# Kernel tuning notes

Measured on AMD Instinct MI355X. Metric: run time of the kernel, lower is better.

## Reference

```python
import jax, jax.numpy as jnp
import numpy as np

K = 3        # kernel_size
STRIDE = 1
PAD = 1
DIL = 1


def conv2d(x, w, b, stride, pad):
    y = jax.lax.conv_general_dilated(
        x, w, window_strides=(stride, stride),
        padding=[(pad, pad), (pad, pad)],
        dimension_numbers=('NCHW', 'OIHW', 'NCHW'))
    return y + b[None, :, None, None]


def bilinear_sample(x_t, py, px):
    """x_t: [B,H,W,C]; py,px: [B,Ho,Wo] float sample coords. Zero padding outside."""
    B, H, W, C = x_t.shape
    b = jnp.arange(B)[:, None, None]
    y0 = jnp.floor(py)
    x0 = jnp.floor(px)
    wy = py - y0
    wx = px - x0
    out = jnp.zeros(py.shape + (C,), x_t.dtype)
    for dy, dx, wgt in ((0, 0, (1 - wy) * (1 - wx)),
                        (0, 1, (1 - wy) * wx),
                        (1, 0, wy * (1 - wx)),
                        (1, 1, wy * wx)):
        yy = y0 + dy
        xx = x0 + dx
        valid = (yy >= 0) & (yy < H) & (xx >= 0) & (xx < W)
        yi = jnp.clip(yy, 0, H - 1).astype(jnp.int32)
        xi = jnp.clip(xx, 0, W - 1).astype(jnp.int32)
        g = x_t[b, yi, xi]                      # [B,Ho,Wo,C] gather
        out = out + g * (wgt * valid)[..., None]
    return out


def deform_conv2d(x, offset, weight, bias):
    """torchvision-style deform_conv2d (v1, 1 offset group).
    x: [B,C,H,W]; offset: [B,2*K*K,Ho,Wo] with (dy,dx) interleaved per tap;
    weight: [O,C,K,K]; bias: [O]."""
    B, C, H, W = x.shape
    O = weight.shape[0]
    Ho, Wo = offset.shape[2], offset.shape[3]
    x_t = jnp.transpose(x, (0, 2, 3, 1))        # [B,H,W,C]
    off = offset.reshape(B, K * K, 2, Ho, Wo)   # [B,K2,(dy,dx),Ho,Wo]
    base_y = (jnp.arange(Ho) * STRIDE - PAD).astype(x.dtype)
    base_x = (jnp.arange(Wo) * STRIDE - PAD).astype(x.dtype)
    samples = []
    for k in range(K * K):                      # fixed 9-tap loop
        ki, kj = divmod(k, K)
        py = base_y[None, :, None] + ki * DIL + off[:, k, 0]   # [B,Ho,Wo]
        px = base_x[None, None, :] + kj * DIL + off[:, k, 1]
        samples.append(bilinear_sample(x_t, py, px))
    sampled = jnp.stack(samples)                # [K2,B,Ho,Wo,C]
    out = jnp.einsum('kbhwc,ock->bohw', sampled, weight.reshape(O, C, K * K))
    return out + bias[None, :, None, None]


def setup_inputs() -> dict:
    key = jax.random.key(0)
    k0, k1, k2, k3 = jax.random.split(key, 4)
    B, Cin, Cout, H, W = 8, 64, 64, 128, 128
    x = jax.random.normal(k0, (B, Cin, H, W), jnp.float32)
    # offset conv: small init so sampled offsets stay near the regular grid
    w_off = jax.random.normal(k1, (2 * K * K, Cin, K, K), jnp.float32) * 0.01
    b_off = jnp.zeros((2 * K * K,), jnp.float32)
    w = jax.random.normal(k2, (Cout, Cin, K, K), jnp.float32) * (1.0 / np.sqrt(Cin * K * K))
    b = jax.random.normal(k3, (Cout,), jnp.float32) * 0.01
    return {"x": x, "w_off": w_off, "b_off": b_off, "w": w, "b": b}


def reference(x, w_off, b_off, w, b):
    offset = conv2d(x, w_off, b_off, STRIDE, PAD)   # [B,18,Ho,Wo]
    return deform_conv2d(x, offset, w, b)           # [B,64,Ho,Wo]
```

## Files before the change

kernel.cpp:

```cpp
#include <hip/hip_runtime.h>

#define B_   8
#define C_   64
#define O_   64
#define H_   128
#define W_   128
#define HO_  128
#define WO_  128
#define K2_  9
#define MOFF 18
#define PLANE (H_*W_)
#define KTOT 576

#define BROWS 5
#define BCOLS 132
#define PSTRIDE (BROWS*BCOLS*8)

typedef short bf16x8 __attribute__((ext_vector_type(8)));
typedef float f32x16 __attribute__((ext_vector_type(16)));
typedef float f32x2  __attribute__((ext_vector_type(2)));
typedef unsigned int u32x4 __attribute__((ext_vector_type(4)));

__device__ __forceinline__ unsigned short f2bf(float f) {
    unsigned u = __float_as_uint(f);
    u += 0x7fff + ((u >> 16) & 1);
    return (unsigned short)(u >> 16);
}
__device__ __forceinline__ float bf2f(short v) {
    return __uint_as_float(((unsigned)(unsigned short)v) << 16);
}
__device__ __forceinline__ f32x2 unpk(unsigned w) {
    f32x2 r;
    r.x = __uint_as_float(w << 16);
    r.y = __uint_as_float(w & 0xffff0000u);
    return r;
}

__global__ __launch_bounds__(256) void prep_kernel(const float* __restrict__ x,
                                                   const float* __restrict__ w,
                                                   const float* __restrict__ w_off,
                                                   unsigned short* __restrict__ xt,
                                                   unsigned short* __restrict__ wbf) {
    __shared__ unsigned short T[64 * 130];
    const int tid = threadIdx.x;
    if (blockIdx.x >= B_ * H_) {
        int i = (blockIdx.x - B_ * H_) * 256 + tid;
        if (i < 96 * KTOT) {
            int o = i / KTOT, pos = i % KTOT;
            int cc = pos / 144, r = pos % 144, t = r / 16, cl = r % 16;
            int c = cc * 16 + cl;
            unsigned short v;
            if (o < O_)             v = f2bf(w[o * KTOT + c * 9 + t]);
            else if (o < O_ + MOFF) v = f2bf(w_off[(o - O_) * KTOT + c * 9 + t]);
            else                    v = 0;
            wbf[i] = v;
        }
        return;
    }
    const int b = blockIdx.x & 7;
    const int y = blockIdx.x >> 3;
    const float* src = x + (size_t)b * C_ * PLANE + y * W_;
    for (int i = tid; i < 64 * 128; i += 256) {
        int c = i >> 7, px = i & 127;
        T[c * 130 + px] = f2bf(src[c * PLANE + px]);
    }
    __syncthreads();
    for (int j = tid; j < 128 * 4; j += 256) {
        int cc = j >> 7, px = j & 127;
        unsigned short* dst = xt + ((size_t)(cc * B_ + b) * PLANE + y * W_ + px) * 16;
        ushort4 v0 = { T[(cc*16+ 0)*130+px], T[(cc*16+ 1)*130+px],
                       T[(cc*16+ 2)*130+px], T[(cc*16+ 3)*130+px] };
        ushort4 v1 = { T[(cc*16+ 4)*130+px], T[(cc*16+ 5)*130+px],
                       T[(cc*16+ 6)*130+px], T[(cc*16+ 7)*130+px] };
        ushort4 v2 = { T[(cc*16+ 8)*130+px], T[(cc*16+ 9)*130+px],
                       T[(cc*16+10)*130+px], T[(cc*16+11)*130+px] };
        ushort4 v3 = { T[(cc*16+12)*130+px], T[(cc*16+13)*130+px],
                       T[(cc*16+14)*130+px], T[(cc*16+15)*130+px] };
        *(ushort4*)(dst)      = v0;
        *(ushort4*)(dst + 4)  = v1;
        *(ushort4*)(dst + 8)  = v2;
        *(ushort4*)(dst + 12) = v3;
    }
}

__global__ __launch_bounds__(256, 4) void fused_kernel(const unsigned short* __restrict__ xt,
        const unsigned short* __restrict__ wobf, const float* __restrict__ b_off,
        const unsigned short* __restrict__ wbf, const float* __restrict__ bias,
        float* __restrict__ out) {
    __shared__ __align__(16) unsigned short band[2 * PSTRIDE];
    __shared__ float lo[MOFF * 128];
    const int tid  = threadIdx.x;
    const int id   = blockIdx.x;
    const int b    = id & 7;
    const int ho   = id >> 3;
    const int wv   = tid >> 6;
    const int lane = tid & 63;
    const int m    = lane & 31;
    const int kh   = lane >> 5;
    const int pxg  = (wv << 5) + m;

    auto stage = [&](const unsigned short* xtc, int r0, int nrows) {
        const int npos = nrows * BCOLS;
        uint4 va[3], vb[3];
        #pragma unroll
        for (int it = 0; it < 3; ++it) {
            va[it] = (uint4){0, 0, 0, 0};
            vb[it] = (uint4){0, 0, 0, 0};
            int j = tid + it * 256;
            if (j < npos) {
                int r = j / BCOLS, c = j - r * BCOLS;
                int y = ho - 2 + r0 + r, x = c - 2;
                if (((unsigned)y < (unsigned)H_) && ((unsigned)x < (unsigned)W_)) {
                    const uint4* gp = (const uint4*)(xtc + (y * W_ + x) * 16);
                    va[it] = gp[0];
                    vb[it] = gp[1];
                }
            }
        }
        #pragma unroll
        for (int it = 0; it < 3; ++it) {
            int j = tid + it * 256;
            if (j < npos) {
                int r = j / BCOLS, c = j - r * BCOLS;
                int s = ((r0 + r) * BCOLS + c) * 8;
                *(uint4*)&band[s]           = va[it];
                *(uint4*)&band[PSTRIDE + s] = vb[it];
            }
        }
    };

    f32x16 acc0 = {};
    for (int cc = 0; cc < 4; ++cc) {
        const unsigned short* xtc = xt + (size_t)(cc * B_ + b) * PLANE * 16;
        stage(xtc, 1, 3);
        __syncthreads();
        #pragma unroll
        for (int ks = 0; ks < 9; ++ks) {
            bf16x8 a = *(const bf16x8*)&wobf[m * KTOT + cc * 144 + ks * 16 + kh * 8];
            bf16x8 s = *(const bf16x8*)&band[kh * PSTRIDE +
                        ((1 + ks / 3) * BCOLS + pxg + ks % 3 + 1) * 8];
            acc0 = __builtin_amdgcn_mfma_f32_32x32x16_bf16(a, s, acc0, 0, 0, 0);
        }
        __syncthreads();
    }
    #pragma unroll
    for (int r = 0; r < 16; ++r) {
        int mo = (r & 3) + ((r >> 2) << 3) + (kh << 2);
        if (mo < MOFF) lo[mo * 128 + pxg] = acc0[r] + b_off[mo];
    }
    __syncthreads();

    f32x16 acc[2] = {};
    for (int cc = 0; cc < 4; ++cc) {
        const unsigned short* xtc = xt + (size_t)(cc * B_ + b) * PLANE * 16;
        stage(xtc, 0, 5);
        __syncthreads();
        #pragma unroll
        for (int ks = 0; ks < 9; ++ks) {
            float py  = (float)(ho - 1 + ks / 3) + lo[(2 * ks) * 128 + pxg];
            float pxc = (float)(pxg - 1 + ks % 3) + lo[(2 * ks + 1) * 128 + pxg];
            float fy = floorf(py), fx = floorf(pxc);
            float wy = py - fy,    wx = pxc - fx;
            int y0 = (int)fy, x0 = (int)fx;
            int rb = y0 - ho + 2, cb = x0 + 2;
            bool oob = ((unsigned)rb > 3u) || ((unsigned)cb > 130u);
            int rbc = min(max(rb, 0), 3), cbc = min(max(cb, 0), 130);
            const unsigned short* bp = &band[kh * PSTRIDE + (rbc * BCOLS + cbc) * 8];
            const uint4 c00 = *(const uint4*)bp;
            const uint4 c01 = *(const uint4*)(bp + 8);
            const uint4 c10 = *(const uint4*)(bp + BCOLS * 8);
            const uint4 c11 = *(const uint4*)(bp + BCOLS * 8 + 8);
            const f32x2 wx2 = { wx, wx };
            const f32x2 wy2 = { wy, wy };
            u32x4 vr;
            #pragma unroll
            for (int pq = 0; pq < 4; ++pq) {
                unsigned w00 = (pq==0)?c00.x:(pq==1)?c00.y:(pq==2)?c00.z:c00.w;
                unsigned w01 = (pq==0)?c01.x:(pq==1)?c01.y:(pq==2)?c01.z:c01.w;
                unsigned w10 = (pq==0)?c10.x:(pq==1)?c10.y:(pq==2)?c10.z:c10.w;
                unsigned w11 = (pq==0)?c11.x:(pq==1)?c11.y:(pq==2)?c11.z:c11.w;
                f32x2 a2 = unpk(w00), b2 = unpk(w01);
                f32x2 c2 = unpk(w10), d2 = unpk(w11);
                f32x2 top = a2 + wx2 * (b2 - a2);
                f32x2 bot = c2 + wx2 * (d2 - c2);
                f32x2 r2  = top + wy2 * (bot - top);
                unsigned pk;
                asm("v_cvt_pk_bf16_f32 %0, %1, %2" : "=v"(pk) : "v"(r2.x), "v"(r2.y));
                vr[pq] = pk;
            }
            bf16x8 v = __builtin_bit_cast(bf16x8, vr);
            if (__builtin_expect(__any(oob), 0)) {
                if (oob) {
                    float s8[8];
                    #pragma unroll
                    for (int j = 0; j < 8; ++j) s8[j] = 0.f;
                    #pragma unroll
                    for (int c2i = 0; c2i < 4; ++c2i) {
                        int yy = y0 + (c2i >> 1);
                        int xx = x0 + (c2i & 1);
                        bool valid = ((unsigned)yy < (unsigned)H_) && ((unsigned)xx < (unsigned)W_);
                        int yc = min(max(yy, 0), H_ - 1);
                        int xc = min(max(xx, 0), W_ - 1);
                        float wgt = ((c2i >> 1) ? wy : 1.f - wy) * ((c2i & 1) ? wx : 1.f - wx);
                        wgt = valid ? wgt : 0.f;
                        const unsigned short* rp = xtc + (yc * W_ + xc) * 16 + kh * 8;
                        bf16x8 u = *(const bf16x8*)rp;
                        #pragma unroll
                        for (int j = 0; j < 8; ++j) s8[j] += wgt * bf2f(u[j]);
                    }
                    #pragma unroll
                    for (int j = 0; j < 8; ++j) v[j] = (short)f2bf(s8[j]);
                }
            }
            bf16x8 a0 = *(const bf16x8*)&wbf[m * KTOT + cc * 144 + ks * 16 + kh * 8];
            bf16x8 a1 = *(const bf16x8*)&wbf[(32 + m) * KTOT + cc * 144 + ks * 16 + kh * 8];
            acc[0] = __builtin_amdgcn_mfma_f32_32x32x16_bf16(a0, v, acc[0], 0, 0, 0);
            acc[1] = __builtin_amdgcn_mfma_f32_32x32x16_bf16(a1, v, acc[1], 0, 0, 0);
        }
        __syncthreads();
    }

    {
        float* op = out + (size_t)b * O_ * PLANE + ho * WO_ + pxg;
        #pragma unroll
        for (int nt = 0; nt < 2; ++nt) {
            #pragma unroll
            for (int r = 0; r < 16; ++r) {
                int mo = (nt << 5) + (r & 3) + ((r >> 2) << 3) + (kh << 2);
                __builtin_nontemporal_store(acc[nt][r] + bias[mo], op + (size_t)mo * PLANE);
            }
        }
    }
}

extern "C" void kernel_launch(void* const* d_in, const int* in_sizes, int n_in,
                              void* d_out, int out_size, void* d_ws, size_t ws_size,
                              hipStream_t stream) {
    const float* x     = (const float*)d_in[0];
    const float* w_off = (const float*)d_in[1];
    const float* b_off = (const float*)d_in[2];
    const float* w     = (const float*)d_in[3];
    const float* bias  = (const float*)d_in[4];
    float* out = (float*)d_out;

    unsigned short* wbf  = (unsigned short*)d_ws;
    unsigned short* wobf = wbf + O_ * KTOT;
    unsigned short* xt   = wobf + 32 * KTOT;

    const int wblocks = (96 * KTOT + 255) / 256;
    prep_kernel <<<B_ * H_ + wblocks, 256, 0, stream>>>(x, w, w_off, xt, wbf);
    fused_kernel<<<B_ * HO_, 256, 0, stream>>>(xt, wobf, b_off, wbf, bias, out);
}
```

Before: 146.3 us.

## Prefetch next channel chunk into registers while MFMA runs; vectorize prep loads

The fused kernel now issues the global loads for the next channel chunk's halo band into registers before computing on the current chunk, then writes them to shared memory at the next iteration. This overlaps global-memory latency with MFMA and bilinear work, including a prefetch of the first deform-phase band during the last offset-conv chunk. The prep kernel reads x as float4 and pads its shared transpose buffer to 132 so the vectorized stores stay aligned. The cost is extra registers held across the compute loop, which may reduce occupancy under the 256x4 launch bound.

```diff
diff --git a/kernel.cpp b/kernel.cpp
--- a/kernel.cpp
+++ b/kernel.cpp
@@ -41,7 +41,7 @@
                                                    const float* __restrict__ w_off,
                                                    unsigned short* __restrict__ xt,
                                                    unsigned short* __restrict__ wbf) {
-    __shared__ unsigned short T[64 * 130];
+    __shared__ __align__(16) unsigned short T[64 * 132];
     const int tid = threadIdx.x;
     if (blockIdx.x >= B_ * H_) {
         int i = (blockIdx.x - B_ * H_) * 256 + tid;
@@ -59,23 +59,25 @@
     }
     const int b = blockIdx.x & 7;
     const int y = blockIdx.x >> 3;
-    const float* src = x + (size_t)b * C_ * PLANE + y * W_;
-    for (int i = tid; i < 64 * 128; i += 256) {
-        int c = i >> 7, px = i & 127;
-        T[c * 130 + px] = f2bf(src[c * PLANE + px]);
+    const float4* src4 = (const float4*)(x + (size_t)b * C_ * PLANE + y * W_);
+    for (int i = tid; i < 64 * 32; i += 256) {
+        int c = i >> 5, px4 = i & 31;
+        float4 v = src4[c * (PLANE / 4) + px4];
+        ushort4 t = { f2bf(v.x), f2bf(v.y), f2bf(v.z), f2bf(v.w) };
+        *(ushort4*)&T[c * 132 + px4 * 4] = t;
     }
     __syncthreads();
     for (int j = tid; j < 128 * 4; j += 256) {
         int cc = j >> 7, px = j & 127;
         unsigned short* dst = xt + ((size_t)(cc * B_ + b) * PLANE + y * W_ + px) * 16;
-        ushort4 v0 = { T[(cc*16+ 0)*130+px], T[(cc*16+ 1)*130+px],
-                       T[(cc*16+ 2)*130+px], T[(cc*16+ 3)*130+px] };
-        ushort4 v1 = { T[(cc*16+ 4)*130+px], T[(cc*16+ 5)*130+px],
-                       T[(cc*16+ 6)*130+px], T[(cc*16+ 7)*130+px] };
-        ushort4 v2 = { T[(cc*16+ 8)*130+px], T[(cc*16+ 9)*130+px],
-                       T[(cc*16+10)*130+px], T[(cc*16+11)*130+px] };
-        ushort4 v3 = { T[(cc*16+12)*130+px], T[(cc*16+13)*130+px],
-                       T[(cc*16+14)*130+px], T[(cc*16+15)*130+px] };
+        ushort4 v0 = { T[(cc*16+ 0)*132+px], T[(cc*16+ 1)*132+px],
+                       T[(cc*16+ 2)*132+px], T[(cc*16+ 3)*132+px] };
+        ushort4 v1 = { T[(cc*16+ 4)*132+px], T[(cc*16+ 5)*132+px],
+                       T[(cc*16+ 6)*132+px], T[(cc*16+ 7)*132+px] };
+        ushort4 v2 = { T[(cc*16+ 8)*132+px], T[(cc*16+ 9)*132+px],
+                       T[(cc*16+10)*132+px], T[(cc*16+11)*132+px] };
+        ushort4 v3 = { T[(cc*16+12)*132+px], T[(cc*16+13)*132+px],
+                       T[(cc*16+14)*132+px], T[(cc*16+15)*132+px] };
         *(ushort4*)(dst)      = v0;
         *(ushort4*)(dst + 4)  = v1;
         *(ushort4*)(dst + 8)  = v2;
@@ -99,41 +101,74 @@
     const int kh   = lane >> 5;
     const int pxg  = (wv << 5) + m;
 
-    auto stage = [&](const unsigned short* xtc, int r0, int nrows) {
-        const int npos = nrows * BCOLS;
-        uint4 va[3], vb[3];
+    uint4 ra[3], rb[3];
+    auto ldA = [&](const unsigned short* xtc) {
+        #pragma unroll
+        for (int it = 0; it < 2; ++it) {
+            ra[it] = (uint4){0, 0, 0, 0};
+            rb[it] = (uint4){0, 0, 0, 0};
+            int j = tid + it * 256;
+            if (j < 3 * BCOLS) {
+                int r = j / BCOLS, c = j - r * BCOLS;
+                int yy = ho - 1 + r, xx = c - 2;
+                if (((unsigned)yy < (unsigned)H_) && ((unsigned)xx < (unsigned)W_)) {
+                    const uint4* gp = (const uint4*)(xtc + (yy * W_ + xx) * 16);
+                    ra[it] = gp[0];
+                    rb[it] = gp[1];
+                }
+            }
+        }
+    };
+    auto stA = [&]() {
+        #pragma unroll
+        for (int it = 0; it < 2; ++it) {
+            int j = tid + it * 256;
+            if (j < 3 * BCOLS) {
+                int r = j / BCOLS, c = j - r * BCOLS;
+                int s = ((1 + r) * BCOLS + c) * 8;
+                *(uint4*)&band[s]           = ra[it];
+                *(uint4*)&band[PSTRIDE + s] = rb[it];
+            }
+        }
+    };
+    auto ldB = [&](const unsigned short* xtc) {
         #pragma unroll
         for (int it = 0; it < 3; ++it) {
-            va[it] = (uint4){0, 0, 0, 0};
-            vb[it] = (uint4){0, 0, 0, 0};
-            int j = tid + it * 256;
-            if (j < npos) {
-                int r = j / BCOLS, c = j - r * BCOLS;
-                int y = ho - 2 + r0 + r, x = c - 2;
-                if (((unsigned)y < (unsigned)H_) && ((unsigned)x < (unsigned)W_)) {
-                    const uint4* gp = (const uint4*)(xtc + (y * W_ + x) * 16);
-                    va[it] = gp[0];
-                    vb[it] = gp[1];
+            ra[it] = (uint4){0, 0, 0, 0};
+            rb[it] = (uint4){0, 0, 0, 0};
+            int j = tid + it * 256;
+            if (j < 5 * BCOLS) {
+                int r = j / BCOLS, c = j - r * BCOLS;
+                int yy = ho - 2 + r, xx = c - 2;
+                if (((unsigned)yy < (unsigned)H_) && ((unsigned)xx < (unsigned)W_)) {
+                    const uint4* gp = (const uint4*)(xtc + (yy * W_ + xx) * 16);
+                    ra[it] = gp[0];
+                    rb[it] = gp[1];
                 }
             }
         }
+    };
+    auto stB = [&]() {
         #pragma unroll
         for (int it = 0; it < 3; ++it) {
             int j = tid + it * 256;
-            if (j < npos) {
-                int r = j / BCOLS, c = j - r * BCOLS;
-                int s = ((r0 + r) * BCOLS + c) * 8;
-                *(uint4*)&band[s]           = va[it];
-                *(uint4*)&band[PSTRIDE + s] = vb[it];
+            if (j < 5 * BCOLS) {
+                int r = j / BCOLS, c = j - r * BCOLS;
+                int s = (r * BCOLS + c) * 8;
+                *(uint4*)&band[s]           = ra[it];
+                *(uint4*)&band[PSTRIDE + s] = rb[it];
             }
         }
     };
 
     f32x16 acc0 = {};
+    ldA(xt + (size_t)(0 * B_ + b) * PLANE * 16);
     for (int cc = 0; cc < 4; ++cc) {
-        const unsigned short* xtc = xt + (size_t)(cc * B_ + b) * PLANE * 16;
-        stage(xtc, 1, 3);
         __syncthreads();
+        stA();
+        __syncthreads();
+        if (cc < 3) ldA(xt + (size_t)((cc + 1) * B_ + b) * PLANE * 16);
+        else        ldB(xt + (size_t)(0 * B_ + b) * PLANE * 16);
         #pragma unroll
         for (int ks = 0; ks < 9; ++ks) {
             bf16x8 a = *(const bf16x8*)&wobf[m * KTOT + cc * 144 + ks * 16 + kh * 8];
@@ -141,7 +176,6 @@
                         ((1 + ks / 3) * BCOLS + pxg + ks % 3 + 1) * 8];
             acc0 = __builtin_amdgcn_mfma_f32_32x32x16_bf16(a, s, acc0, 0, 0, 0);
         }
-        __syncthreads();
     }
     #pragma unroll
     for (int r = 0; r < 16; ++r) {
@@ -153,8 +187,10 @@
     f32x16 acc[2] = {};
     for (int cc = 0; cc < 4; ++cc) {
         const unsigned short* xtc = xt + (size_t)(cc * B_ + b) * PLANE * 16;
-        stage(xtc, 0, 5);
+        if (cc) __syncthreads();
+        stB();
         __syncthreads();
+        if (cc < 3) ldB(xt + (size_t)((cc + 1) * B_ + b) * PLANE * 16);
         #pragma unroll
         for (int ks = 0; ks < 9; ++ks) {
             float py  = (float)(ho - 1 + ks / 3) + lo[(2 * ks) * 128 + pxg];
@@ -162,9 +198,9 @@
             float fy = floorf(py), fx = floorf(pxc);
             float wy = py - fy,    wx = pxc - fx;
             int y0 = (int)fy, x0 = (int)fx;
-            int rb = y0 - ho + 2, cb = x0 + 2;
-            bool oob = ((unsigned)rb > 3u) || ((unsigned)cb > 130u);
-            int rbc = min(max(rb, 0), 3), cbc = min(max(cb, 0), 130);
+            int rb_ = y0 - ho + 2, cb = x0 + 2;
+            bool oob = ((unsigned)rb_ > 3u) || ((unsigned)cb > 130u);
+            int rbc = min(max(rb_, 0), 3), cbc = min(max(cb, 0), 130);
             const unsigned short* bp = &band[kh * PSTRIDE + (rbc * BCOLS + cbc) * 8];
             const uint4 c00 = *(const uint4*)bp;
             const uint4 c01 = *(const uint4*)(bp + 8);
@@ -217,7 +253,6 @@
             acc[0] = __builtin_amdgcn_mfma_f32_32x32x16_bf16(a0, v, acc[0], 0, 0, 0);
             acc[1] = __builtin_amdgcn_mfma_f32_32x32x16_bf16(a1, v, acc[1], 0, 0, 0);
         }
-        __syncthreads();
     }
 
     {
```

Result: no change. 145.2 us (-0.8%).

## Load offset-conv operands from global directly, prefetch next tap, vectorize prep

Applied to the files above, without the earlier changes.

The offset convolution now reads its 9 tap fragments straight from global memory into registers instead of staging a band in LDS, which removes 8 barriers and the stage writes. The main loop software-pipelines the bilinear sampling by computing the next tap's coordinates and LDS loads while the current tap interpolates and feeds the MFMAs. Barriers are reordered so only one sync sits before each restage. The prep kernel reads float4 and writes ushort4 into a 132-padded transpose buffer. This raises register pressure under the 4-waves launch bound and may cause spills.

```diff
diff --git a/kernel.cpp b/kernel.cpp
--- a/kernel.cpp
+++ b/kernel.cpp
@@ -41,7 +41,7 @@
                                                    const float* __restrict__ w_off,
                                                    unsigned short* __restrict__ xt,
                                                    unsigned short* __restrict__ wbf) {
-    __shared__ unsigned short T[64 * 130];
+    __shared__ __align__(16) unsigned short T[64 * 132];
     const int tid = threadIdx.x;
     if (blockIdx.x >= B_ * H_) {
         int i = (blockIdx.x - B_ * H_) * 256 + tid;
@@ -59,23 +59,25 @@
     }
     const int b = blockIdx.x & 7;
     const int y = blockIdx.x >> 3;
-    const float* src = x + (size_t)b * C_ * PLANE + y * W_;
-    for (int i = tid; i < 64 * 128; i += 256) {
-        int c = i >> 7, px = i & 127;
-        T[c * 130 + px] = f2bf(src[c * PLANE + px]);
+    const float4* src4 = (const float4*)(x + (size_t)b * C_ * PLANE + y * W_);
+    for (int i = tid; i < 64 * 32; i += 256) {
+        int c = i >> 5, px4 = i & 31;
+        float4 v = src4[c * (PLANE / 4) + px4];
+        ushort4 t = { f2bf(v.x), f2bf(v.y), f2bf(v.z), f2bf(v.w) };
+        *(ushort4*)&T[c * 132 + px4 * 4] = t;
     }
     __syncthreads();
     for (int j = tid; j < 128 * 4; j += 256) {
         int cc = j >> 7, px = j & 127;
         unsigned short* dst = xt + ((size_t)(cc * B_ + b) * PLANE + y * W_ + px) * 16;
-        ushort4 v0 = { T[(cc*16+ 0)*130+px], T[(cc*16+ 1)*130+px],
-                       T[(cc*16+ 2)*130+px], T[(cc*16+ 3)*130+px] };
-        ushort4 v1 = { T[(cc*16+ 4)*130+px], T[(cc*16+ 5)*130+px],
-                       T[(cc*16+ 6)*130+px], T[(cc*16+ 7)*130+px] };
-        ushort4 v2 = { T[(cc*16+ 8)*130+px], T[(cc*16+ 9)*130+px],
-                       T[(cc*16+10)*130+px], T[(cc*16+11)*130+px] };
-        ushort4 v3 = { T[(cc*16+12)*130+px], T[(cc*16+13)*130+px],
-                       T[(cc*16+14)*130+px], T[(cc*16+15)*130+px] };
+        ushort4 v0 = { T[(cc*16+ 0)*132+px], T[(cc*16+ 1)*132+px],
+                       T[(cc*16+ 2)*132+px], T[(cc*16+ 3)*132+px] };
+        ushort4 v1 = { T[(cc*16+ 4)*132+px], T[(cc*16+ 5)*132+px],
+                       T[(cc*16+ 6)*132+px], T[(cc*16+ 7)*132+px] };
+        ushort4 v2 = { T[(cc*16+ 8)*132+px], T[(cc*16+ 9)*132+px],
+                       T[(cc*16+10)*132+px], T[(cc*16+11)*132+px] };
+        ushort4 v3 = { T[(cc*16+12)*132+px], T[(cc*16+13)*132+px],
+                       T[(cc*16+14)*132+px], T[(cc*16+15)*132+px] };
         *(ushort4*)(dst)      = v0;
         *(ushort4*)(dst + 4)  = v1;
         *(ushort4*)(dst + 8)  = v2;
@@ -99,17 +101,41 @@
     const int kh   = lane >> 5;
     const int pxg  = (wv << 5) + m;
 
-    auto stage = [&](const unsigned short* xtc, int r0, int nrows) {
-        const int npos = nrows * BCOLS;
+    f32x16 acc0 = {};
+    for (int cc = 0; cc < 4; ++cc) {
+        const unsigned short* xtk = xt + (size_t)(cc * B_ + b) * PLANE * 16 + kh * 8;
+        bf16x8 sfr[9];
+        #pragma unroll
+        for (int ks = 0; ks < 9; ++ks) {
+            const int y  = ho - 1 + ks / 3;
+            const int xx = pxg - 1 + ks % 3;
+            bf16x8 s = {};
+            if (((unsigned)y < (unsigned)H_) && ((unsigned)xx < (unsigned)W_))
+                s = *(const bf16x8*)(xtk + (y * W_ + xx) * 16);
+            sfr[ks] = s;
+        }
+        #pragma unroll
+        for (int ks = 0; ks < 9; ++ks) {
+            bf16x8 a = *(const bf16x8*)&wobf[m * KTOT + cc * 144 + ks * 16 + kh * 8];
+            acc0 = __builtin_amdgcn_mfma_f32_32x32x16_bf16(a, sfr[ks], acc0, 0, 0, 0);
+        }
+    }
+    #pragma unroll
+    for (int r = 0; r < 16; ++r) {
+        int mo = (r & 3) + ((r >> 2) << 3) + (kh << 2);
+        if (mo < MOFF) lo[mo * 128 + pxg] = acc0[r] + b_off[mo];
+    }
+
+    auto stage = [&](const unsigned short* xtc) {
         uint4 va[3], vb[3];
         #pragma unroll
         for (int it = 0; it < 3; ++it) {
             va[it] = (uint4){0, 0, 0, 0};
             vb[it] = (uint4){0, 0, 0, 0};
             int j = tid + it * 256;
-            if (j < npos) {
+            if (j < 5 * BCOLS) {
                 int r = j / BCOLS, c = j - r * BCOLS;
-                int y = ho - 2 + r0 + r, x = c - 2;
+                int y = ho - 2 + r, x = c - 2;
                 if (((unsigned)y < (unsigned)H_) && ((unsigned)x < (unsigned)W_)) {
                     const uint4* gp = (const uint4*)(xtc + (y * W_ + x) * 16);
                     va[it] = gp[0];
@@ -120,65 +146,59 @@
         #pragma unroll
         for (int it = 0; it < 3; ++it) {
             int j = tid + it * 256;
-            if (j < npos) {
+            if (j < 5 * BCOLS) {
                 int r = j / BCOLS, c = j - r * BCOLS;
-                int s = ((r0 + r) * BCOLS + c) * 8;
+                int s = (r * BCOLS + c) * 8;
                 *(uint4*)&band[s]           = va[it];
                 *(uint4*)&band[PSTRIDE + s] = vb[it];
             }
         }
     };
 
-    f32x16 acc0 = {};
-    for (int cc = 0; cc < 4; ++cc) {
-        const unsigned short* xtc = xt + (size_t)(cc * B_ + b) * PLANE * 16;
-        stage(xtc, 1, 3);
-        __syncthreads();
-        #pragma unroll
-        for (int ks = 0; ks < 9; ++ks) {
-            bf16x8 a = *(const bf16x8*)&wobf[m * KTOT + cc * 144 + ks * 16 + kh * 8];
-            bf16x8 s = *(const bf16x8*)&band[kh * PSTRIDE +
-                        ((1 + ks / 3) * BCOLS + pxg + ks % 3 + 1) * 8];
-            acc0 = __builtin_amdgcn_mfma_f32_32x32x16_bf16(a, s, acc0, 0, 0, 0);
-        }
-        __syncthreads();
-    }
-    #pragma unroll
-    for (int r = 0; r < 16; ++r) {
-        int mo = (r & 3) + ((r >> 2) << 3) + (kh << 2);
-        if (mo < MOFF) lo[mo * 128 + pxg] = acc0[r] + b_off[mo];
-    }
-    __syncthreads();
+    struct Tap {
+        uint4 c00, c01, c10, c11;
+        float wy, wx;
+        int   y0, x0;
+        int   oob;
+    };
+    auto mk_tap = [&](int ks) {
+        Tap t;
+        float py  = (float)(ho - 1 + ks / 3) + lo[(2 * ks) * 128 + pxg];
+        float pxc = (float)(pxg - 1 + ks % 3) + lo[(2 * ks + 1) * 128 + pxg];
+        float fy = floorf(py), fx = floorf(pxc);
+        t.wy = py - fy;  t.wx = pxc - fx;
+        t.y0 = (int)fy;  t.x0 = (int)fx;
+        int rb_ = t.y0 - ho + 2, cb = t.x0 + 2;
+        t.oob = ((unsigned)rb_ > 3u) || ((unsigned)cb > 130u);
+        int rbc = min(max(rb_, 0), 3), cbc = min(max(cb, 0), 130);
+        const unsigned short* bp = &band[kh * PSTRIDE + (rbc * BCOLS + cbc) * 8];
+        t.c00 = *(const uint4*)bp;
+        t.c01 = *(const uint4*)(bp + 8);
+        t.c10 = *(const uint4*)(bp + BCOLS * 8);
+        t.c11 = *(const uint4*)(bp + BCOLS * 8 + 8);
+        return t;
+    };
 
     f32x16 acc[2] = {};
     for (int cc = 0; cc < 4; ++cc) {
         const unsigned short* xtc = xt + (size_t)(cc * B_ + b) * PLANE * 16;
-        stage(xtc, 0, 5);
+        if (cc) __syncthreads();
+        stage(xtc);
         __syncthreads();
+        Tap cur = mk_tap(0);
         #pragma unroll
         for (int ks = 0; ks < 9; ++ks) {
-            float py  = (float)(ho - 1 + ks / 3) + lo[(2 * ks) * 128 + pxg];
-            float pxc = (float)(pxg - 1 + ks % 3) + lo[(2 * ks + 1) * 128 + pxg];
-            float fy = floorf(py), fx = floorf(pxc);
-            float wy = py - fy,    wx = pxc - fx;
-            int y0 = (int)fy, x0 = (int)fx;
-            int rb = y0 - ho + 2, cb = x0 + 2;
-            bool oob = ((unsigned)rb > 3u) || ((unsigned)cb > 130u);
-            int rbc = min(max(rb, 0), 3), cbc = min(max(cb, 0), 130);
-            const unsigned short* bp = &band[kh * PSTRIDE + (rbc * BCOLS + cbc) * 8];
-            const uint4 c00 = *(const uint4*)bp;
-            const uint4 c01 = *(const uint4*)(bp + 8);
-            const uint4 c10 = *(const uint4*)(bp + BCOLS * 8);
-            const uint4 c11 = *(const uint4*)(bp + BCOLS * 8 + 8);
-            const f32x2 wx2 = { wx, wx };
-            const f32x2 wy2 = { wy, wy };
+            Tap nxt;
+            if (ks < 8) nxt = mk_tap(ks + 1);
+            const f32x2 wx2 = { cur.wx, cur.wx };
+            const f32x2 wy2 = { cur.wy, cur.wy };
             u32x4 vr;
             #pragma unroll
             for (int pq = 0; pq < 4; ++pq) {
-                unsigned w00 = (pq==0)?c00.x:(pq==1)?c00.y:(pq==2)?c00.z:c00.w;
-                unsigned w01 = (pq==0)?c01.x:(pq==1)?c01.y:(pq==2)?c01.z:c01.w;
-                unsigned w10 = (pq==0)?c10.x:(pq==1)?c10.y:(pq==2)?c10.z:c10.w;
-                unsigned w11 = (pq==0)?c11.x:(pq==1)?c11.y:(pq==2)?c11.z:c11.w;
+                unsigned w00 = (pq==0)?cur.c00.x:(pq==1)?cur.c00.y:(pq==2)?cur.c00.z:cur.c00.w;
+                unsigned w01 = (pq==0)?cur.c01.x:(pq==1)?cur.c01.y:(pq==2)?cur.c01.z:cur.c01.w;
+                unsigned w10 = (pq==0)?cur.c10.x:(pq==1)?cur.c10.y:(pq==2)?cur.c10.z:cur.c10.w;
+                unsigned w11 = (pq==0)?cur.c11.x:(pq==1)?cur.c11.y:(pq==2)?cur.c11.z:cur.c11.w;
                 f32x2 a2 = unpk(w00), b2 = unpk(w01);
                 f32x2 c2 = unpk(w10), d2 = unpk(w11);
                 f32x2 top = a2 + wx2 * (b2 - a2);
@@ -189,15 +209,16 @@
                 vr[pq] = pk;
             }
             bf16x8 v = __builtin_bit_cast(bf16x8, vr);
-            if (__builtin_expect(__any(oob), 0)) {
-                if (oob) {
+            if (__builtin_expect(__any(cur.oob), 0)) {
+                if (cur.oob) {
+                    float wy = cur.wy, wx = cur.wx;
                     float s8[8];
                     #pragma unroll
                     for (int j = 0; j < 8; ++j) s8[j] = 0.f;
                     #pragma unroll
                     for (int c2i = 0; c2i < 4; ++c2i) {
-                        int yy = y0 + (c2i >> 1);
-                        int xx = x0 + (c2i & 1);
+                        int yy = cur.y0 + (c2i >> 1);
+                        int xx = cur.x0 + (c2i & 1);
                         bool valid = ((unsigned)yy < (unsigned)H_) && ((unsigned)xx < (unsigned)W_);
                         int yc = min(max(yy, 0), H_ - 1);
                         int xc = min(max(xx, 0), W_ - 1);
@@ -216,8 +237,8 @@
             bf16x8 a1 = *(const bf16x8*)&wbf[(32 + m) * KTOT + cc * 144 + ks * 16 + kh * 8];
             acc[0] = __builtin_amdgcn_mfma_f32_32x32x16_bf16(a0, v, acc[0], 0, 0, 0);
             acc[1] = __builtin_amdgcn_mfma_f32_32x32x16_bf16(a1, v, acc[1], 0, 0, 0);
-        }
-        __syncthreads();
+            if (ks < 8) cur = nxt;
+        }
     }
 
     {
```

After: 149.7 us. 2.3% more time.

## Process two output rows per block and vectorize prep loads

Applied to the files above, without the earlier changes.

The fused kernel now handles two output rows per 512-thread block and stages a 6-row band instead of 5 rows per single row, so each staged halo row is shared by both rows and less staging traffic is spent per output. The prep kernel reads x with float4 loads and writes packed ushort4 to shared memory with a padded stride of 132. The trade-off is larger shared memory per block (bigger band and offset buffer) and 512-thread blocks, which may lower occupancy. Part of the kernel is hidden, so the epilogue's handling of the new row index cannot be checked.

```diff
diff --git a/kernel.cpp b/kernel.cpp
--- a/kernel.cpp
+++ b/kernel.cpp
@@ -12,7 +12,7 @@
 #define PLANE (H_*W_)
 #define KTOT 576
 
-#define BROWS 5
+#define BROWS 6
 #define BCOLS 132
 #define PSTRIDE (BROWS*BCOLS*8)
 
@@ -41,7 +41,7 @@
                                                    const float* __restrict__ w_off,
                                                    unsigned short* __restrict__ xt,
                                                    unsigned short* __restrict__ wbf) {
-    __shared__ unsigned short T[64 * 130];
+    __shared__ __align__(16) unsigned short T[64 * 132];
     const int tid = threadIdx.x;
     if (blockIdx.x >= B_ * H_) {
         int i = (blockIdx.x - B_ * H_) * 256 + tid;
@@ -59,23 +59,25 @@
     }
     const int b = blockIdx.x & 7;
     const int y = blockIdx.x >> 3;
-    const float* src = x + (size_t)b * C_ * PLANE + y * W_;
-    for (int i = tid; i < 64 * 128; i += 256) {
-        int c = i >> 7, px = i & 127;
-        T[c * 130 + px] = f2bf(src[c * PLANE + px]);
+    const float4* src4 = (const float4*)(x + (size_t)b * C_ * PLANE + y * W_);
+    for (int i = tid; i < 64 * 32; i += 256) {
+        int c = i >> 5, px4 = i & 31;
+        float4 v = src4[c * (PLANE / 4) + px4];
+        ushort4 t = { f2bf(v.x), f2bf(v.y), f2bf(v.z), f2bf(v.w) };
+        *(ushort4*)&T[c * 132 + px4 * 4] = t;
     }
     __syncthreads();
     for (int j = tid; j < 128 * 4; j += 256) {
         int cc = j >> 7, px = j & 127;
         unsigned short* dst = xt + ((size_t)(cc * B_ + b) * PLANE + y * W_ + px) * 16;
-        ushort4 v0 = { T[(cc*16+ 0)*130+px], T[(cc*16+ 1)*130+px],
-                       T[(cc*16+ 2)*130+px], T[(cc*16+ 3)*130+px] };
-        ushort4 v1 = { T[(cc*16+ 4)*130+px], T[(cc*16+ 5)*130+px],
-                       T[(cc*16+ 6)*130+px], T[(cc*16+ 7)*130+px] };
-        ushort4 v2 = { T[(cc*16+ 8)*130+px], T[(cc*16+ 9)*130+px],
-                       T[(cc*16+10)*130+px], T[(cc*16+11)*130+px] };
-        ushort4 v3 = { T[(cc*16+12)*130+px], T[(cc*16+13)*130+px],
-                       T[(cc*16+14)*130+px], T[(cc*16+15)*130+px] };
+        ushort4 v0 = { T[(cc*16+ 0)*132+px], T[(cc*16+ 1)*132+px],
+                       T[(cc*16+ 2)*132+px], T[(cc*16+ 3)*132+px] };
+        ushort4 v1 = { T[(cc*16+ 4)*132+px], T[(cc*16+ 5)*132+px],
+                       T[(cc*16+ 6)*132+px], T[(cc*16+ 7)*132+px] };
+        ushort4 v2 = { T[(cc*16+ 8)*132+px], T[(cc*16+ 9)*132+px],
+                       T[(cc*16+10)*132+px], T[(cc*16+11)*132+px] };
+        ushort4 v3 = { T[(cc*16+12)*132+px], T[(cc*16+13)*132+px],
+                       T[(cc*16+14)*132+px], T[(cc*16+15)*132+px] };
         *(ushort4*)(dst)      = v0;
         *(ushort4*)(dst + 4)  = v1;
         *(ushort4*)(dst + 8)  = v2;
@@ -83,33 +85,35 @@
     }
 }
 
-__global__ __launch_bounds__(256, 4) void fused_kernel(const unsigned short* __restrict__ xt,
+__global__ __launch_bounds__(512, 4) void fused_kernel(const unsigned short* __restrict__ xt,
         const unsigned short* __restrict__ wobf, const float* __restrict__ b_off,
         const unsigned short* __restrict__ wbf, const float* __restrict__ bias,
         float* __restrict__ out) {
     __shared__ __align__(16) unsigned short band[2 * PSTRIDE];
-    __shared__ float lo[MOFF * 128];
+    __shared__ float lo[MOFF * 256];
     const int tid  = threadIdx.x;
     const int id   = blockIdx.x;
     const int b    = id & 7;
-    const int ho   = id >> 3;
+    const int r0   = (id >> 3) << 1;
     const int wv   = tid >> 6;
+    const int rl   = wv >> 2;
+    const int ho   = r0 + rl;
     const int lane = tid & 63;
     const int m    = lane & 31;
     const int kh   = lane >> 5;
-    const int pxg  = (wv << 5) + m;
-
-    auto stage = [&](const unsigned short* xtc, int r0, int nrows) {
+    const int pxg  = ((wv & 3) << 5) + m;
+
+    auto stage = [&](const unsigned short* xtc, int ybase, int nrows) {
         const int npos = nrows * BCOLS;
-        uint4 va[3], vb[3];
-        #pragma unroll
-        for (int it = 0; it < 3; ++it) {
+        uint4 va[2], vb[2];
+        #pragma unroll
+        for (int it = 0; it < 2; ++it) {
             va[it] = (uint4){0, 0, 0, 0};
             vb[it] = (uint4){0, 0, 0, 0};
-            int j = tid + it * 256;
+            int j = tid + it * 512;
             if (j < npos) {
                 int r = j / BCOLS, c = j - r * BCOLS;
-                int y = ho - 2 + r0 + r, x = c - 2;
+                int y = ybase + r, x = c - 2;
                 if (((unsigned)y < (unsigned)H_) && ((unsigned)x < (unsigned)W_)) {
                     const uint4* gp = (const uint4*)(xtc + (y * W_ + x) * 16);
                     va[it] = gp[0];
@@ -118,11 +122,11 @@
             }
         }
         #pragma unroll
-        for (int it = 0; it < 3; ++it) {
-            int j = tid + it * 256;
+        for (int it = 0; it < 2; ++it) {
+            int j = tid + it * 512;
             if (j < npos) {
                 int r = j / BCOLS, c = j - r * BCOLS;
-                int s = ((r0 + r) * BCOLS + c) * 8;
+                int s = (r * BCOLS + c) * 8;
                 *(uint4*)&band[s]           = va[it];
                 *(uint4*)&band[PSTRIDE + s] = vb[it];
             }
@@ -132,13 +136,13 @@
     f32x16 acc0 = {};
     for (int cc = 0; cc < 4; ++cc) {
         const unsigned short* xtc = xt + (size_t)(cc * B_ + b) * PLANE * 16;
-        stage(xtc, 1, 3);
+        stage(xtc, r0 - 1, 4);
         __syncthreads();
         #pragma unroll
         for (int ks = 0; ks < 9; ++ks) {
             bf16x8 a = *(const bf16x8*)&wobf[m * KTOT + cc * 144 + ks * 16 + kh * 8];
             bf16x8 s = *(const bf16x8*)&band[kh * PSTRIDE +
-                        ((1 + ks / 3) * BCOLS + pxg + ks % 3 + 1) * 8];
+                        ((rl + ks / 3) * BCOLS + pxg + ks % 3 + 1) * 8];
             acc0 = __builtin_amdgcn_mfma_f32_32x32x16_bf16(a, s, acc0, 0, 0, 0);
         }
         __syncthreads();
@@ -146,25 +150,25 @@
     #pragma unroll
     for (int r = 0; r < 16; ++r) {
         int mo = (r & 3) + ((r >> 2) << 3) + (kh << 2);
-        if (mo < MOFF) lo[mo * 128 + pxg] = acc0[r] + b_off[mo];
+        if (mo < MOFF) lo[mo * 256 + rl * 128 + pxg] = acc0[r] + b_off[mo];
     }
     __syncthreads();
 
     f32x16 acc[2] = {};
     for (int cc = 0; cc < 4; ++cc) {
         const unsigned short* xtc = xt + (size_t)(cc * B_ + b) * PLANE * 16;
-        stage(xtc, 0, 5);
+        stage(xtc, r0 - 2, 6);
         __syncthreads();
         #pragma unroll
         for (int ks = 0; ks < 9; ++ks) {
-            float py  = (float)(ho - 1 + ks / 3) + lo[(2 * ks) * 128 + pxg];
-            float pxc = (float)(pxg - 1 + ks % 3) + lo[(2 * ks + 1) * 128 + pxg];
+            float py  = (float)(ho - 1 + ks / 3) + lo[(2 * ks) * 256 + rl * 128 + pxg];
+            float pxc = (float)(pxg - 1 + ks % 3) + lo[(2 * ks + 1) * 256 + rl * 128 + pxg];
             float fy = floorf(py), fx = floorf(pxc);
             float wy = py - fy,    wx = pxc - fx;
             int y0 = (int)fy, x0 = (int)fx;
-            int rb = y0 - ho + 2, cb = x0 + 2;
-            bool oob = ((unsigned)rb > 3u) || ((unsigned)cb > 130u);
-            int rbc = min(max(rb, 0), 3), cbc = min(max(cb, 0), 130);
+            int rb_ = y0 - r0 + 2, cb = x0 + 2;
+            bool oob = ((unsigned)rb_ > 4u) || ((unsigned)cb > 130u);
+            int rbc = min(max(rb_, 0), 4), cbc = min(max(cb, 0), 130);
             const unsigned short* bp = &band[kh * PSTRIDE + (rbc * BCOLS + cbc) * 8];
             const uint4 c00 = *(const uint4*)bp;
             const uint4 c01 = *(const uint4*)(bp + 8);
@@ -249,5 +253,5 @@
 
     const int wblocks = (96 * KTOT + 255) / 256;
     prep_kernel <<<B_ * H_ + wblocks, 256, 0, stream>>>(x, w, w_off, xt, wbf);
-    fused_kernel<<<B_ * HO_, 256, 0, stream>>>(xt, wobf, b_off, wbf, bias, out);
-}
+    fused_kernel<<<B_ * HO_ / 2, 512, 0, stream>>>(xt, wobf, b_off, wbf, bias, out);
+}
```

After: 144.6 us (median of 2 runs). No clear change (-1.2%).
